# Kernel tuning notes

Hardware: AMD Instinct MI355X
Metric: run time of the kernel (lower is better)

Reference implementation:

```python
import jax, jax.numpy as jnp
import numpy as np

B, S, V, D, G, H, L, K = 32, 256, 100000, 128, 128, 256, 32, 3
ALPHA = 0.5


def lstm_pass(x, mask, W, U, b, reverse):
    # x: (B,S,I), mask: (B,S) bool. PyTorch gate order i,f,g,o.
    Bh = x.shape[0]
    Hd = U.shape[0]
    h0 = jnp.zeros((Bh, Hd), x.dtype)
    c0 = jnp.zeros((Bh, Hd), x.dtype)

    def step(carry, inp):
        h, c = carry
        xt, mt = inp
        g = xt @ W + h @ U + b
        i, f, gg, o = jnp.split(g, 4, axis=-1)
        i = jax.nn.sigmoid(i)
        f = jax.nn.sigmoid(f)
        gg = jnp.tanh(gg)
        o = jax.nn.sigmoid(o)
        cn = f * c + i * gg
        hn = o * jnp.tanh(cn)
        m = mt[:, None]
        h = jnp.where(m, hn, h)
        c = jnp.where(m, cn, c)
        return (h, c), h * m.astype(h.dtype)

    _, hs = jax.lax.scan(step, (h0, c0), (x.transpose(1, 0, 2), mask.T), reverse=reverse)
    return hs.transpose(1, 0, 2)  # (B,S,Hd), zero at padded steps (like pad_packed)


def setup_inputs() -> dict:
    key = jax.random.key(0)
    ks = jax.random.split(key, 24)
    word_inputs = jax.random.randint(ks[0], (B, S), 0, V)
    lens = jnp.sort(jax.random.randint(ks[1], (B,), S // 2, S + 1))[::-1]
    mask = (jnp.arange(S)[None, :] < lens[:, None])
    idx_inputs = jax.random.randint(ks[2], (B, S), 0, V)
    char_inputs = jax.random.randint(ks[3], (B * S, 4), 0, 100)
    char_seq_lengths = jnp.ones((B * S,), jnp.int64 if jax.config.jax_enable_x64 else jnp.int32)
    char_seq_recover = jnp.arange(B * S)
    s = lambda k, sh, sc: jax.random.normal(k, sh, jnp.float32) * sc
    I = D + G
    inp = {
        'word_inputs': word_inputs,
        'word_seq_lengths': lens,
        'char_inputs': char_inputs,
        'char_seq_lengths': char_seq_lengths,
        'char_seq_recover': char_seq_recover,
        'mask': mask,
        'idx_inputs': idx_inputs,
        'word_embedding': s(ks[4], (V, D), 0.1),
        'label_embedding': s(ks[5], (L, D), 0.1),
        'sent_W': s(ks[6], (D, G), 1.0 / np.sqrt(D)),
        'sent_b': jnp.zeros((G,), jnp.float32),
        'conv_W': s(ks[7], (L, L, K), 1.0 / np.sqrt(L * K)),
        'conv_b': jnp.zeros((L,), jnp.float32),
        'lstm_Wf': s(ks[8], (I, 4 * H // 2), 1.0 / np.sqrt(I)),
        'lstm_Uf': s(ks[9], (H // 2, 4 * H // 2), 1.0 / np.sqrt(H // 2)),
        'lstm_bf': jnp.zeros((4 * H // 2,), jnp.float32),
        'lstm_Wb': s(ks[10], (I, 4 * H // 2), 1.0 / np.sqrt(I)),
        'lstm_Ub': s(ks[11], (H // 2, 4 * H // 2), 1.0 / np.sqrt(H // 2)),
        'lstm_bb': jnp.zeros((4 * H // 2,), jnp.float32),
        'tag_W': s(ks[12], (H, L), 1.0 / np.sqrt(H)),
        'tag_b': jnp.zeros((L,), jnp.float32),
        'mem_W': s(ks[13], (H, L), 1.0 / np.sqrt(H)),
        'mem_b': jnp.zeros((L,), jnp.float32),
        'mem_bank': s(ks[14], (V, H), 0.1),
    }
    return inp


def reference(word_inputs, word_seq_lengths, char_inputs, char_seq_lengths, char_seq_recover,
              mask, idx_inputs, word_embedding, label_embedding, sent_W, sent_b,
              conv_W, conv_b, lstm_Wf, lstm_Uf, lstm_bf, lstm_Wb, lstm_Ub, lstm_bb,
              tag_W, tag_b, mem_W, mem_b, mem_bank):
    maskf = mask.astype(jnp.float32)
    # ---- WordRep: embeddings + label cosine similarity ----
    we = word_embedding[word_inputs]  # (B,S,D) gather
    wn = we / (jnp.linalg.norm(we, axis=-1, keepdims=True) + 1e-8)
    ln = label_embedding / (jnp.linalg.norm(label_embedding, axis=-1, keepdims=True) + 1e-8)
    label_embs = jnp.einsum('bsd,ld->bsl', wn, ln)  # (B,S,L)
    # ---- SentenceRep (projection stand-in) + label attention pooling ----
    sent_hidden = jnp.tanh(we @ sent_W + sent_b)  # (B,S,G)
    lf = jax.lax.conv_general_dilated(
        label_embs.transpose(0, 2, 1), conv_W, (1,), [(K // 2, K // 2)],
        dimension_numbers=('NCH', 'OIH', 'NCH')) + conv_b[None, :, None]
    lf = jax.nn.relu(lf).transpose(0, 2, 1)  # (B,S,L)
    lm = lf.max(axis=-1)  # (B,S)
    # partial (masked) softmax, exactly as in the torch code
    e = jnp.exp(lm) * maskf
    attn = e / e.sum(axis=1, keepdims=True)
    sent_rep = jnp.einsum('bs,bsg->bg', attn, sent_hidden)[:, None, :]  # bmm
    sent_rep = jnp.broadcast_to(sent_rep, (B, S, G))  # repeat over seq
    # ---- BiLSTM over concat(word, sentence) ----
    wr = jnp.concatenate([we, sent_rep], axis=-1)  # (B,S,D+G)
    hf = lstm_pass(wr, mask, lstm_Wf, lstm_Uf, lstm_bf, False)
    hb = lstm_pass(wr, mask, lstm_Wb, lstm_Ub, lstm_bb, True)
    feat = jnp.concatenate([hf, hb], axis=-1)  # (B,S,H)
    outputs = feat @ tag_W + tag_b  # (B,S,L)
    # ---- MemoryBank: gather keyed by word id, zero padded positions ----
    doc_h = mem_bank[word_inputs] * maskf[..., None]  # (B,S,H) irregular gather
    doc_rep = doc_h @ mem_W + mem_b  # mem2tag
    # bank update (side effect in torch; computed functionally, not returned)
    new_bank = mem_bank.at[idx_inputs.reshape(-1)].set(
        (feat * maskf[..., None]).reshape(-1, H))
    del new_bank
    return outputs * (1.0 - ALPHA) + doc_rep * ALPHA
```

## Files before the change

### kernel.cpp

```cpp
#include <hip/hip_runtime.h>
#include <hip/hip_bf16.h>

#define BB 32
#define SS 256
#define DD 128
#define GG 128
#define NG 512
#define LL 32
#define LOG2E 1.4426950408889634f

typedef unsigned short u16;
typedef __attribute__((ext_vector_type(8))) short short8;
typedef __attribute__((ext_vector_type(4))) float f32x4;

__device__ __forceinline__ float bf2f(u16 u){ return __uint_as_float(((unsigned)u)<<16); }
__device__ __forceinline__ u16 f2bf(float f){
    unsigned x = __float_as_uint(f);
    unsigned r = x + 0x7fffu + ((x>>16)&1u);
    return (u16)(r>>16);
}
__device__ __forceinline__ float tanh_f(float x){ float e=__expf(2.0f*x); return 1.0f - 2.0f/(e+1.0f); }

__device__ __forceinline__ float exp2_f(float x){
#if __has_builtin(__builtin_amdgcn_exp2f)
    return __builtin_amdgcn_exp2f(x);
#elif __has_builtin(__builtin_amdgcn_expf)
    return __builtin_amdgcn_expf(x);
#else
    return __expf(x * 0.6931471805599453f);
#endif
}
__device__ __forceinline__ float rcp_f(float x){
#if __has_builtin(__builtin_amdgcn_rcpf)
    return __builtin_amdgcn_rcpf(x);
#else
    return 1.0f / x;
#endif
}

struct PJobs { const void* src[21]; int n[21]; int p0[21]; int p1[21]; int type[21]; };

__global__ void kprep(PJobs jb, const void* __restrict__ wemb, int* __restrict__ flags,
                      float* __restrict__ can,
                      u16* __restrict__ WcatT, u16* __restrict__ tagWT, u16* __restrict__ memWT){
    int t = threadIdx.x;
    __shared__ int cw[4];
    __shared__ int sflag;
    {
        u16 v = ((const u16*)wemb)[2*t];
        int e = (v>>7)&0xFF;
        int c = (e>=0x90)?1:0;
        #pragma unroll
        for (int mk=32; mk>0; mk>>=1) c += __shfl_xor(c, mk);
        if ((t&63)==0) cw[t>>6] = c;
        __syncthreads();
        if (t==0) sflag = (cw[0]+cw[1]+cw[2]+cw[3] >= 32) ? 1 : 0;
        __syncthreads();
    }
    int f = sflag;
    if (blockIdx.x==0 && blockIdx.y==0 && t==0) flags[0] = f;

    int id = blockIdx.y;
    int i = blockIdx.x*256 + t;
    if (i >= jb.n[id]) return;
    const void* src = jb.src[id];
    int p0 = jb.p0[id];
    int ty = jb.type[id];
    if (ty == 0){
        float v = f ? ((const float*)src)[i] : bf2f(((const u16*)src)[i]);
        can[p0 + i] = v;
    } else if (ty == 1){
        int c = i>>7, k = i&127;
        float v = f ? ((const float*)src)[k*jb.p1[id] + c] : bf2f(((const u16*)src)[k*jb.p1[id] + c]);
        WcatT[(size_t)(p0 + c)*128 + k] = f2bf(v);
    } else if (ty == 2){
        int l = i&31, k = i>>5;
        float v = f ? ((const float*)src)[k*32 + l] : bf2f(((const u16*)src)[k*32 + l]);
        (p0 ? memWT : tagWT)[l*256 + k] = f2bf(v);
    } else if (ty == 3){
        int row = i>>7, col = i&127;
        float v = f ? ((const float*)src)[i] : bf2f(((const u16*)src)[i]);
        float sq = v*v;
        #pragma unroll
        for (int mk=32; mk>0; mk>>=1) sq += __shfl_xor(sq, mk);
        __shared__ float r4[4];
        if ((t&63)==0) r4[t>>6] = sq;
        __syncthreads();
        int half = t>>7;
        float tot = r4[half*2] + r4[half*2+1];
        float inv = 1.0f/(sqrtf(tot) + 1e-8f);
        WcatT[(size_t)(1152+row)*128 + col] = f2bf(v*inv);
        WcatT[(size_t)(1184+row)*128 + col] = 0;
    } else {
        int c = i>>7, k = i&127;
        float v = f ? ((const float*)src)[k*512 + c] : bf2f(((const u16*)src)[k*512 + c]);
        int q = c>>7, rem = c&127, w5 = rem>>4, li = rem&15;
        WcatT[(size_t)(p0 + w5*64 + q*16 + li)*128 + k] = f2bf(v);
    }
}

__global__ __launch_bounds__(256) void k1_token(const int* __restrict__ wid,
                         const void* __restrict__ wemb,
                         const int* __restrict__ flags,
                         u16* __restrict__ weC, float* __restrict__ invn){
    int t = threadIdx.x;
    int tl = t>>5, lane = t&31;
    int tok = blockIdx.x*8 + tl;
    int idx = wid[tok];
    float v0,v1,v2,v3;
    if (flags[0]){
        f32x4 u = *(const f32x4*)((const float*)wemb + (size_t)idx*DD + lane*4);
        v0=u[0]; v1=u[1]; v2=u[2]; v3=u[3];
    } else {
        ushort4 u = *(const ushort4*)((const u16*)wemb + (size_t)idx*DD + lane*4);
        v0=bf2f(u.x); v1=bf2f(u.y); v2=bf2f(u.z); v3=bf2f(u.w);
    }
    int b = tok>>8, s = tok&255;
    int m = s*BB + b;
    ushort4 wv;
    wv.x=f2bf(v0); wv.y=f2bf(v1); wv.z=f2bf(v2); wv.w=f2bf(v3);
    *(ushort4*)&weC[(size_t)m*DD + lane*4] = wv;
    float sq = v0*v0 + v1*v1 + v2*v2 + v3*v3;
    #pragma unroll
    for (int mk=16; mk>0; mk>>=1) sq += __shfl_xor(sq, mk);
    if (lane==0) invn[m] = 1.0f/(sqrtf(sq) + 1e-8f);
}

__global__ __launch_bounds__(256) void kgemm(const u16* __restrict__ weC,
                      const u16* __restrict__ WcatT,
                      const float* __restrict__ invn, const float* __restrict__ sentBc,
                      float* __restrict__ gpre4, float* __restrict__ sent_h,
                      float* __restrict__ lab_e){
    int mt = blockIdx.x;
    int nb = blockIdx.y;
    int t = threadIdx.x;
    int w4 = t>>6, l = t&63, li = l&15, lg = l>>4;
    int mbase = mt*64 + w4*16;
    int n0 = nb*64;
    short8 af[4];
    #pragma unroll
    for (int ks=0;ks<4;ks++)
        af[ks] = *(const short8*)&weC[(size_t)(mbase + li)*128 + ks*32 + lg*8];
    f32x4 acc[4];
    #pragma unroll
    for (int nt=0;nt<4;nt++){
        short8 bf[4];
        #pragma unroll
        for (int ks=0;ks<4;ks++)
            bf[ks] = *(const short8*)&WcatT[(size_t)(n0 + nt*16 + li)*128 + ks*32 + lg*8];
        f32x4 a; a[0]=0.f; a[1]=0.f; a[2]=0.f; a[3]=0.f;
        #pragma unroll
        for (int ks=0;ks<4;ks++)
            a = __builtin_amdgcn_mfma_f32_16x16x32_bf16(af[ks], bf[ks], a, 0,0,0);
        acc[nt] = a;
    }
    if (nb < 16){
        int dir = nb>>3, w5 = nb&7;
        int s = mt*2 + (w4>>1);
        int bg = (w4&1)*4 + lg;
        float* gp = gpre4 + ((((size_t)(dir*8+bg)*256 + s)*8 + w5)*256);
        #pragma unroll
        for (int r=0;r<4;r++){
            f32x4 v;
            v[0] = acc[0][r]*LOG2E;
            v[1] = acc[1][r]*LOG2E;
            v[2] = acc[2][r]*(2.0f*LOG2E);
            v[3] = acc[3][r]*LOG2E;
            *(f32x4*)&gp[(r*16 + li)*4] = v;
        }
    } else {
        int mrow = mbase + lg*4;
        #pragma unroll
        for (int nt=0;nt<4;nt++){
            int n = n0 + nt*16 + li;
            if (n < 1152){
                int c = n - 1024;
                float bb = sentBc[c];
                #pragma unroll
                for (int r=0;r<4;r++){
                    int m = mrow + r;
                    int b = m&31, s = m>>5;
                    sent_h[((size_t)(b*256+s))*128 + c] = tanh_f(acc[nt][r] + bb);
                }
            } else if (n < 1184){
                int c = n - 1152;
                #pragma unroll
                for (int r=0;r<4;r++){
                    int m = mrow + r;
                    int b = m&31, s = m>>5;
                    lab_e[((size_t)(b*256+s))*32 + c] = acc[nt][r] * invn[m];
                }
            }
        }
    }
}

__global__ __launch_bounds__(256) void k23p(const float* __restrict__ lab_e,
                        const float* __restrict__ convWc, const float* __restrict__ convBc,
                        const float* __restrict__ sent_h,
                        const int* __restrict__ lens,
                        float* __restrict__ srp, float* __restrict__ esum_p){
    int b = blockIdx.x, stile = blockIdx.y, t = threadIdx.x;
    int sl = t>>3, oq = t&7;
    int s = stile*32 + sl;
    __shared__ float le_s[34*33];
    __shared__ float wle[LL*LL*3];
    __shared__ float wb[LL];
    __shared__ float es[32];
    __shared__ float red[2][GG];
    int s0 = stile*32;
    for (int i=t; i<34*32; i+=256){
        int row = i>>5, col = i&31;
        int sg = s0 - 1 + row;
        le_s[row*33 + col] = (sg>=0 && sg<SS) ? lab_e[(size_t)b*SS*LL + sg*LL + col] : 0.f;
    }
    for (int i=t; i<LL*LL*3; i+=256) wle[i] = convWc[i];
    if (t < LL) wb[t] = convBc[t];
    __syncthreads();
    float lm = 0.f;
    #pragma unroll
    for (int op=0; op<4; op++){
        int o = oq*4 + op;
        float a0 = wb[o], a1 = 0.f, a2 = 0.f;
        #pragma unroll
        for (int i=0;i<LL;i++){
            a0 = fmaf(le_s[(sl+0)*33+i], wle[o*96 + i*3    ], a0);
            a1 = fmaf(le_s[(sl+1)*33+i], wle[o*96 + i*3 + 1], a1);
            a2 = fmaf(le_s[(sl+2)*33+i], wle[o*96 + i*3 + 2], a2);
        }
        lm = fmaxf(lm, fmaxf(a0+a1+a2, 0.f));
    }
    #pragma unroll
    for (int mk=1; mk<8; mk<<=1) lm = fmaxf(lm, __shfl_xor(lm, mk));
    if (oq == 0) es[sl] = (s < lens[b]) ? __expf(lm) : 0.f;
    __syncthreads();
    int col = t&127, sh = t>>7;
    float a0 = 0.f, a1 = 0.f;
    int sb = s0 + sh*16;
    #pragma unroll
    for (int s2=0; s2<16; s2+=2){
        a0 = fmaf(es[sh*16+s2],   sent_h[((size_t)b*SS + sb+s2)*GG + col], a0);
        a1 = fmaf(es[sh*16+s2+1], sent_h[((size_t)b*SS + sb+s2+1)*GG + col], a1);
    }
    red[sh][col] = a0+a1;
    __syncthreads();
    if (t < GG) srp[((size_t)b*8 + stile)*GG + t] = red[0][t] + red[1][t];
    if (t < 32){
        float e = es[t];
        #pragma unroll
        for (int mk=16; mk>0; mk>>=1) e += __shfl_xor(e, mk);
        if (t==0) esum_p[b*8 + stile] = e;
    }
}

__global__ void k3b_cpart(const float* __restrict__ srp, const float* __restrict__ esum_p,
                          const float* __restrict__ Wfc, const float* __restrict__ Wbc,
                          const float* __restrict__ bfc, const float* __restrict__ bbc,
                          float* __restrict__ cpart){
    int chunk = blockIdx.x, b = blockIdx.y, t = threadIdx.x;
    __shared__ float srs[GG];
    if (t < GG){
        float a = 0.f;
        #pragma unroll
        for (int st=0; st<8; st++) a += srp[((size_t)b*8 + st)*GG + t];
        float es = 0.f;
        #pragma unroll
        for (int st=0; st<8; st++) es += esum_p[b*8 + st];
        srs[t] = a * (1.0f/es);
    }
    __syncthreads();
    int ng = chunk*256 + t;
    int dir = ng>>9, n = ng&511;
    const float* W = dir ? Wbc : Wfc;
    float c0 = (dir ? bbc : bfc)[n], c1 = 0.f;
    for (int g=0; g<GG; g+=2){
        c0 = fmaf(srs[g],   W[(size_t)(DD+g)*NG + n], c0);
        c1 = fmaf(srs[g+1], W[(size_t)(DD+g+1)*NG + n], c1);
    }
    cpart[((size_t)dir*NG + n)*BB + b] = c0+c1;
}

__global__ __launch_bounds__(512) void k5_lstm(const float* __restrict__ gpre4,
                       const float* __restrict__ Ufc, const float* __restrict__ Ubc,
                       const float* __restrict__ cpart,
                       const int* __restrict__ lens, float* __restrict__ feat){
    int dir = blockIdx.x>>3, bg = blockIdx.x&7;
    int t = threadIdx.x;
    int w = t>>6, l = t&63, lg = l>>4, li = l&15;
    int j = w*16 + li;
    int b = bg*4 + lg;
    const float* Uc = dir ? Ubc : Ufc;

    short8 bfr[4][4];
    #pragma unroll
    for (int q=0;q<4;q++){
        float sc = (q==2) ? 2.0f*LOG2E : LOG2E;
        #pragma unroll
        for (int ks=0;ks<4;ks++){
            int n = q*128 + j;
            short8 v;
            #pragma unroll
            for (int jj=0;jj<8;jj++)
                v[jj] = (short)f2bf(Uc[(size_t)(ks*32 + lg*8 + jj)*NG + n] * sc);
            bfr[q][ks] = v;
        }
    }
    float cpr[4];
    #pragma unroll
    for (int q=0;q<4;q++)
        cpr[q] = cpart[((size_t)(dir*NG + q*128 + j))*BB + b] * ((q==2) ? 2.0f*LOG2E : LOG2E);
    int len1 = lens[b];

    __shared__ u16 Hhi[2][16*128];
    for (int i=t; i<2*2048; i+=512) ((u16*)Hhi)[i] = 0;

    bool rdp = ((li & 3) == 0);
    int roff[4];
    #pragma unroll
    for (int ks=0;ks<4;ks++)
        roff[ks] = (li*256 + ((ks*64 + lg*16) ^ ((li&7)<<4))) >> 1;
    int woff;
    { int row = lg*4; woff = (row*256 + ((2*j) ^ ((row&7)<<4))) >> 1; }

    short8 ah[4];
    #pragma unroll
    for (int ks=0;ks<4;ks++){
        #pragma unroll
        for (int jj=0;jj<8;jj++) ah[ks][jj] = 0;
    }
    f32x4 acv[4];
    #pragma unroll
    for (int q=0;q<4;q++){ acv[q][0]=0.f; acv[q][1]=0.f; acv[q][2]=0.f; acv[q][3]=0.f; }

    float c = 0.f, h = 0.f;
    int sgn = dir ? -1 : 1;
    int s0 = dir ? (SS-1) : 0;
    const float* gl = gpre4 + ((size_t)(dir*8 + bg)*256 + s0)*2048 + w*256 + l*4;
    ptrdiff_t gstep = (ptrdiff_t)sgn * 2048;

    f32x4 gA = *(const f32x4*)gl;
    f32x4 gB = *(const f32x4*)(gl + gstep);
    const float* glp = gl + 2*gstep;

    float* fb = feat + ((size_t)b*SS + s0)*256 + dir*128 + j;
    ptrdiff_t fstep = (ptrdiff_t)sgn * 256;

    int s = s0;
    __syncthreads();

#define K5_STEP(P, G)                                                          \
    {                                                                          \
        if (rdp){                                                              \
            ah[0] = *(const short8*)&Hhi[P][roff[0]];                          \
            ah[1] = *(const short8*)&Hhi[P][roff[1]];                          \
            ah[2] = *(const short8*)&Hhi[P][roff[2]];                          \
            ah[3] = *(const short8*)&Hhi[P][roff[3]];                          \
        }                                                                      \
        acv[0][0] = G[0]+cpr[0];                                               \
        acv[1][0] = G[1]+cpr[1];                                               \
        acv[2][0] = G[2]+cpr[2];                                               \
        acv[3][0] = G[3]+cpr[3];                                               \
        if (tt2 + 2 < SS){ G = *(const f32x4*)glp; glp += gstep; }             \
        _Pragma("unroll")                                                      \
        for (int ks=0;ks<4;ks++){                                              \
            _Pragma("unroll")                                                  \
            for (int q=0;q<4;q++)                                              \
                acv[q] = __builtin_amdgcn_mfma_f32_16x16x32_bf16(ah[ks], bfr[q][ks], acv[q], 0,0,0); \
        }                                                                      \
        float si = rcp_f(1.0f + exp2_f(-acv[0][0]));                           \
        float sf = rcp_f(1.0f + exp2_f(-acv[1][0]));                           \
        float tg = 1.0f - 2.0f*rcp_f(exp2_f(acv[2][0]) + 1.0f);                \
        float so = rcp_f(1.0f + exp2_f(-acv[3][0]));                           \
        float cn = sf*c + si*tg;                                               \
        float th = 1.0f - 2.0f*rcp_f(exp2_f(cn*(2.0f*LOG2E)) + 1.0f);          \
        float hn = so*th;                                                      \
        if (s < 128){ c = cn; h = hn; fb[0] = hn; }                            \
        else { bool mm = (s < len1); c = mm?cn:c; h = mm?hn:h; fb[0] = mm?hn:0.f; } \
        Hhi[P^1][woff] = f2bf(h);                                              \
        asm volatile("s_waitcnt lgkmcnt(0)" ::: "memory");                     \
        __builtin_amdgcn_sched_barrier(0);                                     \
        __builtin_amdgcn_s_barrier();                                          \
        __builtin_amdgcn_sched_barrier(0);                                     \
        s += sgn; fb += fstep;                                                 \
    }

    for (int tt=0; tt<SS; tt+=2){
        { int tt2 = tt;   K5_STEP(0, gA) }
        { int tt2 = tt+1; K5_STEP(1, gB) }
    }
#undef K5_STEP
}

__global__ __launch_bounds__(256) void k6_final(const float* __restrict__ feat,
                         const int* __restrict__ wid,
                         const int* __restrict__ lens,
                         const u16* __restrict__ tagWT, const float* __restrict__ tagBc,
                         const u16* __restrict__ memWT, const float* __restrict__ memBc,
                         const void* __restrict__ bank, const int* __restrict__ flags,
                         void* __restrict__ out){
    int t = threadIdx.x;
    int tl = t>>5, lcol = t&31;
    int tok0 = blockIdx.x*8;
    __shared__ float fr_s[8][256];
    __shared__ float br_s[8][256];
    __shared__ int idxs[8];
    __shared__ int msks[8];
    if (t < 8){
        int tok = tok0 + t;
        idxs[t] = wid[tok];
        msks[t] = ((tok&255) < lens[tok>>8]) ? 1 : 0;
    }
    __syncthreads();
    int f32m = flags[0];
    {
        const float* fp = feat + (size_t)(tok0+tl)*256 + lcol*8;
        f32x4 u0 = *(const f32x4*)fp;
        f32x4 u1 = *(const f32x4*)(fp+4);
        *(f32x4*)&fr_s[tl][lcol*8]   = u0;
        *(f32x4*)&fr_s[tl][lcol*8+4] = u1;
    }
    if (msks[tl]){
        if (f32m){
            const float* bp = (const float*)bank + (size_t)idxs[tl]*256 + lcol*8;
            f32x4 u0 = *(const f32x4*)bp;
            f32x4 u1 = *(const f32x4*)(bp+4);
            *(f32x4*)&br_s[tl][lcol*8]   = u0;
            *(f32x4*)&br_s[tl][lcol*8+4] = u1;
        } else {
            short8 bv = *(const short8*)((const u16*)bank + (size_t)idxs[tl]*256 + lcol*8);
            #pragma unroll
            for (int e=0;e<8;e++) br_s[tl][lcol*8+e] = bf2f((u16)bv[e]);
        }
    } else {
        #pragma unroll
        for (int e=0;e<8;e++) br_s[tl][lcol*8+e] = 0.f;
    }
    __syncthreads();
    float a0 = tagBc[lcol], a1=0.f, a2=0.f, a3=0.f;
    float b0 = memBc[lcol], b1=0.f, b2=0.f, b3=0.f;
    #pragma unroll 4
    for (int cc=0; cc<32; cc++){
        short8 tw = *(const short8*)&tagWT[lcol*256 + cc*8];
        short8 mw = *(const short8*)&memWT[lcol*256 + cc*8];
        f32x4 f0 = *(const f32x4*)&fr_s[tl][cc*8];
        f32x4 f1 = *(const f32x4*)&fr_s[tl][cc*8+4];
        f32x4 g0 = *(const f32x4*)&br_s[tl][cc*8];
        f32x4 g1 = *(const f32x4*)&br_s[tl][cc*8+4];
        a0 = fmaf(f0[0], bf2f((u16)tw[0]), a0);
        a1 = fmaf(f0[1], bf2f((u16)tw[1]), a1);
        a2 = fmaf(f0[2], bf2f((u16)tw[2]), a2);
        a3 = fmaf(f0[3], bf2f((u16)tw[3]), a3);
        a0 = fmaf(f1[0], bf2f((u16)tw[4]), a0);
        a1 = fmaf(f1[1], bf2f((u16)tw[5]), a1);
        a2 = fmaf(f1[2], bf2f((u16)tw[6]), a2);
        a3 = fmaf(f1[3], bf2f((u16)tw[7]), a3);
        b0 = fmaf(g0[0], bf2f((u16)mw[0]), b0);
        b1 = fmaf(g0[1], bf2f((u16)mw[1]), b1);
        b2 = fmaf(g0[2], bf2f((u16)mw[2]), b2);
        b3 = fmaf(g0[3], bf2f((u16)mw[3]), b3);
        b0 = fmaf(g1[0], bf2f((u16)mw[4]), b0);
        b1 = fmaf(g1[1], bf2f((u16)mw[5]), b1);
        b2 = fmaf(g1[2], bf2f((u16)mw[6]), b2);
        b3 = fmaf(g1[3], bf2f((u16)mw[7]), b3);
    }
    float r1 = (a0+a1)+(a2+a3);
    float r2 = (b0+b1)+(b2+b3);
    float res = 0.5f*r1 + 0.5f*r2;
    int tok = tok0 + tl;
    if (f32m) ((float*)out)[(size_t)tok*LL + lcol] = res;
    else      ((u16*)out)[(size_t)tok*LL + lcol]   = f2bf(res);
}

extern "C" void kernel_launch(void* const* d_in, const int* in_sizes, int n_in,
                              void* d_out, int out_size, void* d_ws, size_t ws_size,
                              hipStream_t stream){
    const int* wid  = (const int*)d_in[0];
    const int* lens = (const int*)d_in[1];

    char* ws = (char*)d_ws;
    int*   flags  = (int*)  (ws + 0);
    float* can    = (float*)(ws + 1024);
    u16*   WcatT  = (u16*)  (ws + 1900544);
    u16*   tagWT  = (u16*)  (ws + 2211840);
    u16*   memWT  = (u16*)  (ws + 2228224);
    float* invn   = (float*)(ws + 2244608);
    float* cpart  = (float*)(ws + 2277376);
    float* srp    = (float*)(ws + 2441216);
    float* esum_p = (float*)(ws + 2572288);
    u16*   weC    = (u16*)  (ws + 4194304);
    float* lab_e  = (float*)(ws + 8388608);
    float* sent_h = (float*)(ws + 9437184);
    float* gpre4  = (float*)(ws + 16777216);
    float* feat   = (float*)(ws + 50331648);

    float* sentBc = can + 20480;
    float* convWc = can + 20608;
    float* convBc = can + 23680;
    float* Wfc    = can + 23712;
    float* Wbc    = can + 154784;
    float* bfc    = can + 285856;
    float* bbc    = can + 286368;
    float* Ufc    = can + 286880;
    float* Ubc    = can + 352416;
    float* tagBc  = can + 426144;
    float* memBc  = can + 434368;

    static const int cn_n[15]   = {4096,16384,128,3072,32,131072,131072,512,512,65536,65536,8192,32,8192,32};
    static const int cn_src[15] = {8,9,10,11,12,13,16,15,18,14,17,19,20,21,22};
    PJobs jb;
    {
        int off = 0;
        for (int i=0;i<15;i++){
            jb.src[i]=d_in[cn_src[i]]; jb.n[i]=cn_n[i]; jb.p0[i]=off; jb.p1[i]=0; jb.type[i]=0;
            off+=cn_n[i];
        }
        jb.src[15]=d_in[13]; jb.n[15]=65536; jb.p0[15]=0;    jb.p1[15]=512; jb.type[15]=4;
        jb.src[16]=d_in[16]; jb.n[16]=65536; jb.p0[16]=512;  jb.p1[16]=512; jb.type[16]=4;
        jb.src[17]=d_in[9];  jb.n[17]=16384; jb.p0[17]=1024; jb.p1[17]=128; jb.type[17]=1;
        jb.src[18]=d_in[19]; jb.n[18]=8192;  jb.p0[18]=0;    jb.p1[18]=0;   jb.type[18]=2;
        jb.src[19]=d_in[21]; jb.n[19]=8192;  jb.p0[19]=1;    jb.p1[19]=0;   jb.type[19]=2;
        jb.src[20]=d_in[8];  jb.n[20]=4096;  jb.p0[20]=0;    jb.p1[20]=0;   jb.type[20]=3;
    }

    kprep  <<<dim3(512,21), 256, 0, stream>>>(jb, d_in[7], flags, can, WcatT, tagWT, memWT);
    k1_token<<<1024, 256, 0, stream>>>(wid, d_in[7], flags, weC, invn);
    kgemm  <<<dim3(128,19), 256, 0, stream>>>(weC, WcatT, invn, sentBc, gpre4, sent_h, lab_e);
    k23p   <<<dim3(32,8), 256, 0, stream>>>(lab_e, convWc, convBc, sent_h, lens, srp, esum_p);
    k3b_cpart<<<dim3(4,32), 256, 0, stream>>>(srp, esum_p, Wfc, Wbc, bfc, bbc, cpart);
    k5_lstm<<<16, 512, 0, stream>>>(gpre4, Ufc, Ubc, cpart, lens, feat);
    k6_final<<<1024, 256, 0, stream>>>(feat, wid, lens, tagWT, tagBc, memWT, memBc,
                                       d_in[23], flags, d_out);
}
```

Baseline: 209.8 us.

## Store LSTM gate preactivations in bf16 and fold token embedding into prep kernel

The precomputed LSTM input projections (gpre4) are now written and read as bf16 instead of fp32, halving the memory the GEMM writes and the serial LSTM kernel streams each step. Separately, the token-embedding gather/normalize kernel is merged into the prep kernel as an extra job, and the 2D launch grid is replaced by a flat grid with per-job block offsets so no blocks are launched empty. This removes one launch and the idle blocks, but the bf16 gate values lose precision in the recurrence.

```diff
diff --git a/kernel.cpp b/kernel.cpp
--- a/kernel.cpp
+++ b/kernel.cpp
@@ -38,11 +38,14 @@
 #endif
 }
 
-struct PJobs { const void* src[21]; int n[21]; int p0[21]; int p1[21]; int type[21]; };
-
-__global__ void kprep(PJobs jb, const void* __restrict__ wemb, int* __restrict__ flags,
-                      float* __restrict__ can,
-                      u16* __restrict__ WcatT, u16* __restrict__ tagWT, u16* __restrict__ memWT){
+#define NJOBS 22
+struct PJobs { const void* src[NJOBS]; int n[NJOBS]; int p0[NJOBS]; int p1[NJOBS];
+               int type[NJOBS]; int blk0[NJOBS]; };
+
+__global__ void kprep(PJobs jb, const void* __restrict__ wemb, const int* __restrict__ wid,
+                      int* __restrict__ flags, float* __restrict__ can,
+                      u16* __restrict__ WcatT, u16* __restrict__ tagWT, u16* __restrict__ memWT,
+                      u16* __restrict__ weC, float* __restrict__ invn){
     int t = threadIdx.x;
     __shared__ int cw[4];
     __shared__ int sflag;
@@ -58,10 +61,13 @@
         __syncthreads();
     }
     int f = sflag;
-    if (blockIdx.x==0 && blockIdx.y==0 && t==0) flags[0] = f;
-
-    int id = blockIdx.y;
-    int i = blockIdx.x*256 + t;
+    if (blockIdx.x==0 && t==0) flags[0] = f;
+
+    int bx = blockIdx.x;
+    int id = 0;
+    #pragma unroll
+    for (int jj=1; jj<NJOBS; jj++) if (bx >= jb.blk0[jj]) id = jj;
+    int i = (bx - jb.blk0[id])*256 + t;
     if (i >= jb.n[id]) return;
     const void* src = jb.src[id];
     int p0 = jb.p0[id];
@@ -91,45 +97,38 @@
         float inv = 1.0f/(sqrtf(tot) + 1e-8f);
         WcatT[(size_t)(1152+row)*128 + col] = f2bf(v*inv);
         WcatT[(size_t)(1184+row)*128 + col] = 0;
-    } else {
+    } else if (ty == 4){
         int c = i>>7, k = i&127;
         float v = f ? ((const float*)src)[k*512 + c] : bf2f(((const u16*)src)[k*512 + c]);
         int q = c>>7, rem = c&127, w5 = rem>>4, li = rem&15;
         WcatT[(size_t)(p0 + w5*64 + q*16 + li)*128 + k] = f2bf(v);
-    }
-}
-
-__global__ __launch_bounds__(256) void k1_token(const int* __restrict__ wid,
-                         const void* __restrict__ wemb,
-                         const int* __restrict__ flags,
-                         u16* __restrict__ weC, float* __restrict__ invn){
-    int t = threadIdx.x;
-    int tl = t>>5, lane = t&31;
-    int tok = blockIdx.x*8 + tl;
-    int idx = wid[tok];
-    float v0,v1,v2,v3;
-    if (flags[0]){
-        f32x4 u = *(const f32x4*)((const float*)wemb + (size_t)idx*DD + lane*4);
-        v0=u[0]; v1=u[1]; v2=u[2]; v3=u[3];
     } else {
-        ushort4 u = *(const ushort4*)((const u16*)wemb + (size_t)idx*DD + lane*4);
-        v0=bf2f(u.x); v1=bf2f(u.y); v2=bf2f(u.z); v3=bf2f(u.w);
-    }
-    int b = tok>>8, s = tok&255;
-    int m = s*BB + b;
-    ushort4 wv;
-    wv.x=f2bf(v0); wv.y=f2bf(v1); wv.z=f2bf(v2); wv.w=f2bf(v3);
-    *(ushort4*)&weC[(size_t)m*DD + lane*4] = wv;
-    float sq = v0*v0 + v1*v1 + v2*v2 + v3*v3;
-    #pragma unroll
-    for (int mk=16; mk>0; mk>>=1) sq += __shfl_xor(sq, mk);
-    if (lane==0) invn[m] = 1.0f/(sqrtf(sq) + 1e-8f);
+        int tok = i>>5, lane = i&31;
+        int idx = wid[tok];
+        float v0,v1,v2,v3;
+        if (f){
+            f32x4 u = *(const f32x4*)((const float*)wemb + (size_t)idx*DD + lane*4);
+            v0=u[0]; v1=u[1]; v2=u[2]; v3=u[3];
+        } else {
+            ushort4 u = *(const ushort4*)((const u16*)wemb + (size_t)idx*DD + lane*4);
+            v0=bf2f(u.x); v1=bf2f(u.y); v2=bf2f(u.z); v3=bf2f(u.w);
+        }
+        int b = tok>>8, s = tok&255;
+        int m = s*BB + b;
+        ushort4 wv;
+        wv.x=f2bf(v0); wv.y=f2bf(v1); wv.z=f2bf(v2); wv.w=f2bf(v3);
+        *(ushort4*)&weC[(size_t)m*DD + lane*4] = wv;
+        float sq = v0*v0 + v1*v1 + v2*v2 + v3*v3;
+        #pragma unroll
+        for (int mk=16; mk>0; mk>>=1) sq += __shfl_xor(sq, mk);
+        if (lane==0) invn[m] = 1.0f/(sqrtf(sq) + 1e-8f);
+    }
 }
 
 __global__ __launch_bounds__(256) void kgemm(const u16* __restrict__ weC,
                       const u16* __restrict__ WcatT,
                       const float* __restrict__ invn, const float* __restrict__ sentBc,
-                      float* __restrict__ gpre4, float* __restrict__ sent_h,
+                      u16* __restrict__ gpre4, float* __restrict__ sent_h,
                       float* __restrict__ lab_e){
     int mt = blockIdx.x;
     int nb = blockIdx.y;
@@ -158,15 +157,15 @@
         int dir = nb>>3, w5 = nb&7;
         int s = mt*2 + (w4>>1);
         int bg = (w4&1)*4 + lg;
-        float* gp = gpre4 + ((((size_t)(dir*8+bg)*256 + s)*8 + w5)*256);
+        u16* gp = gpre4 + ((((size_t)(dir*8+bg)*256 + s)*8 + w5)*256);
         #pragma unroll
         for (int r=0;r<4;r++){
-            f32x4 v;
-            v[0] = acc[0][r]*LOG2E;
-            v[1] = acc[1][r]*LOG2E;
-            v[2] = acc[2][r]*(2.0f*LOG2E);
-            v[3] = acc[3][r]*LOG2E;
-            *(f32x4*)&gp[(r*16 + li)*4] = v;
+            ushort4 v;
+            v.x = f2bf(acc[0][r]*LOG2E);
+            v.y = f2bf(acc[1][r]*LOG2E);
+            v.z = f2bf(acc[2][r]*(2.0f*LOG2E));
+            v.w = f2bf(acc[3][r]*LOG2E);
+            *(ushort4*)&gp[(r*16 + li)*4] = v;
         }
     } else {
         int mrow = mbase + lg*4;
@@ -280,7 +279,7 @@
     cpart[((size_t)dir*NG + n)*BB + b] = c0+c1;
 }
 
-__global__ __launch_bounds__(512) void k5_lstm(const float* __restrict__ gpre4,
+__global__ __launch_bounds__(512) void k5_lstm(const u16* __restrict__ gpre4,
                        const float* __restrict__ Ufc, const float* __restrict__ Ubc,
                        const float* __restrict__ cpart,
                        const int* __restrict__ lens, float* __restrict__ feat){
@@ -335,12 +334,12 @@
     float c = 0.f, h = 0.f;
     int sgn = dir ? -1 : 1;
     int s0 = dir ? (SS-1) : 0;
-    const float* gl = gpre4 + ((size_t)(dir*8 + bg)*256 + s0)*2048 + w*256 + l*4;
+    const u16* gl = gpre4 + ((size_t)(dir*8 + bg)*256 + s0)*2048 + w*256 + l*4;
     ptrdiff_t gstep = (ptrdiff_t)sgn * 2048;
 
-    f32x4 gA = *(const f32x4*)gl;
-    f32x4 gB = *(const f32x4*)(gl + gstep);
-    const float* glp = gl + 2*gstep;
+    ushort4 gA = *(const ushort4*)gl;
+    ushort4 gB = *(const ushort4*)(gl + gstep);
+    const u16* glp = gl + 2*gstep;
 
     float* fb = feat + ((size_t)b*SS + s0)*256 + dir*128 + j;
     ptrdiff_t fstep = (ptrdiff_t)sgn * 256;
@@ -356,11 +355,11 @@
             ah[2] = *(const short8*)&Hhi[P][roff[2]];                          \
             ah[3] = *(const short8*)&Hhi[P][roff[3]];                          \
         }                                                                      \
-        acv[0][0] = G[0]+cpr[0];                                               \
-        acv[1][0] = G[1]+cpr[1];                                               \
-        acv[2][0] = G[2]+cpr[2];                                               \
-        acv[3][0] = G[3]+cpr[3];                                               \
-        if (tt2 + 2 < SS){ G = *(const f32x4*)glp; glp += gstep; }             \
+        acv[0][0] = bf2f(G.x)+cpr[0];                                          \
+        acv[1][0] = bf2f(G.y)+cpr[1];                                          \
+        acv[2][0] = bf2f(G.z)+cpr[2];                                          \
+        acv[3][0] = bf2f(G.w)+cpr[3];                                          \
+        if (tt2 + 2 < SS){ G = *(const ushort4*)glp; glp += gstep; }           \
         _Pragma("unroll")                                                      \
         for (int ks=0;ks<4;ks++){                                              \
             _Pragma("unroll")                                                  \
@@ -490,7 +489,7 @@
     u16*   weC    = (u16*)  (ws + 4194304);
     float* lab_e  = (float*)(ws + 8388608);
     float* sent_h = (float*)(ws + 9437184);
-    float* gpre4  = (float*)(ws + 16777216);
+    u16*   gpre4  = (u16*)  (ws + 16777216);
     float* feat   = (float*)(ws + 50331648);
 
     float* sentBc = can + 20480;
@@ -508,22 +507,25 @@
     static const int cn_n[15]   = {4096,16384,128,3072,32,131072,131072,512,512,65536,65536,8192,32,8192,32};
     static const int cn_src[15] = {8,9,10,11,12,13,16,15,18,14,17,19,20,21,22};
     PJobs jb;
+    int nblk = 0;
     {
         int off = 0;
         for (int i=0;i<15;i++){
             jb.src[i]=d_in[cn_src[i]]; jb.n[i]=cn_n[i]; jb.p0[i]=off; jb.p1[i]=0; jb.type[i]=0;
             off+=cn_n[i];
         }
-        jb.src[15]=d_in[13]; jb.n[15]=65536; jb.p0[15]=0;    jb.p1[15]=512; jb.type[15]=4;
-        jb.src[16]=d_in[16]; jb.n[16]=65536; jb.p0[16]=512;  jb.p1[16]=512; jb.type[16]=4;
-        jb.src[17]=d_in[9];  jb.n[17]=16384; jb.p0[17]=1024; jb.p1[17]=128; jb.type[17]=1;
-        jb.src[18]=d_in[19]; jb.n[18]=8192;  jb.p0[18]=0;    jb.p1[18]=0;   jb.type[18]=2;
-        jb.src[19]=d_in[21]; jb.n[19]=8192;  jb.p0[19]=1;    jb.p1[19]=0;   jb.type[19]=2;
-        jb.src[20]=d_in[8];  jb.n[20]=4096;  jb.p0[20]=0;    jb.p1[20]=0;   jb.type[20]=3;
-    }
-
-    kprep  <<<dim3(512,21), 256, 0, stream>>>(jb, d_in[7], flags, can, WcatT, tagWT, memWT);
-    k1_token<<<1024, 256, 0, stream>>>(wid, d_in[7], flags, weC, invn);
+        jb.src[15]=d_in[13]; jb.n[15]=65536;  jb.p0[15]=0;    jb.p1[15]=512; jb.type[15]=4;
+        jb.src[16]=d_in[16]; jb.n[16]=65536;  jb.p0[16]=512;  jb.p1[16]=512; jb.type[16]=4;
+        jb.src[17]=d_in[9];  jb.n[17]=16384;  jb.p0[17]=1024; jb.p1[17]=128; jb.type[17]=1;
+        jb.src[18]=d_in[19]; jb.n[18]=8192;   jb.p0[18]=0;    jb.p1[18]=0;   jb.type[18]=2;
+        jb.src[19]=d_in[21]; jb.n[19]=8192;   jb.p0[19]=1;    jb.p1[19]=0;   jb.type[19]=2;
+        jb.src[20]=d_in[8];  jb.n[20]=4096;   jb.p0[20]=0;    jb.p1[20]=0;   jb.type[20]=3;
+        jb.src[21]=d_in[7];  jb.n[21]=262144; jb.p0[21]=0;    jb.p1[21]=0;   jb.type[21]=5;
+        for (int i=0;i<NJOBS;i++){ jb.blk0[i] = nblk; nblk += (jb.n[i] + 255)/256; }
+    }
+
+    kprep  <<<nblk, 256, 0, stream>>>(jb, d_in[7], wid, flags, can, WcatT, tagWT, memWT,
+                                      weC, invn);
     kgemm  <<<dim3(128,19), 256, 0, stream>>>(weC, WcatT, invn, sentBc, gpre4, sent_h, lab_e);
     k23p   <<<dim3(32,8), 256, 0, stream>>>(lab_e, convWc, convBc, sent_h, lens, srp, esum_p);
     k3b_cpart<<<dim3(4,32), 256, 0, stream>>>(srp, esum_p, Wfc, Wbc, bfc, bbc, cpart);
```

After: 215.5 us. 1.03x slower.
